# Performance work log

Hardware: AMD Instinct MI355X
Metric: run time of the kernel (lower is better)

## Reference

```python
import jax, jax.numpy as jnp
import numpy as np

N = 50000
E = 800000
IN_C = 256
NHID = 32
HEADS = 4
OUT_C = 64
HID = NHID * HEADS  # 128
SLOPE = 0.2


def setup_inputs() -> dict:
    key = jax.random.key(0)
    ks = jax.random.split(key, 16)
    s = lambda *d: 1.0 / np.sqrt(d[0])
    inp = {
        "x": jax.random.normal(ks[0], (N, IN_C), dtype=jnp.float32),
        "edge_index": jax.random.randint(ks[1], (2, E), 0, N, dtype=jnp.int64),
        # conv1: GATConv(IN_C, NHID, heads=HEADS, concat=True)
        "W1": jax.random.normal(ks[2], (IN_C, HEADS * NHID), dtype=jnp.float32) * s(IN_C),
        "att_src1": jax.random.normal(ks[3], (HEADS, NHID), dtype=jnp.float32) * s(NHID),
        "att_dst1": jax.random.normal(ks[4], (HEADS, NHID), dtype=jnp.float32) * s(NHID),
        "b1": jnp.zeros((HEADS * NHID,), dtype=jnp.float32),
        # conv2: GATConv(HID, OUT_C, heads=1, concat=False)
        "W2": jax.random.normal(ks[5], (HID, OUT_C), dtype=jnp.float32) * s(HID),
        "att_src2": jax.random.normal(ks[6], (1, OUT_C), dtype=jnp.float32) * s(OUT_C),
        "att_dst2": jax.random.normal(ks[7], (1, OUT_C), dtype=jnp.float32) * s(OUT_C),
        "b2": jnp.zeros((OUT_C,), dtype=jnp.float32),
        # res1: Linear(IN_C, HID)
        "res1_w": jax.random.normal(ks[8], (IN_C, HID), dtype=jnp.float32) * s(IN_C),
        "res1_b": jnp.zeros((HID,), dtype=jnp.float32),
        # fc: Linear(HID, OUT_C)
        "fc_w": jax.random.normal(ks[9], (HID, OUT_C), dtype=jnp.float32) * s(HID),
        "fc_b": jnp.zeros((OUT_C,), dtype=jnp.float32),
    }
    return inp


def leaky_relu(x, slope=SLOPE):
    return jnp.where(x >= 0, x, slope * x)


def gat_conv(x, edge_index, W, att_src, att_dst, bias, heads, out_c, concat):
    """PyG GATConv with default add_self_loops=True, negative_slope=0.2."""
    n = x.shape[0]
    loop = jnp.arange(n, dtype=edge_index.dtype)
    src = jnp.concatenate([edge_index[0], loop])  # [E+N]
    dst = jnp.concatenate([edge_index[1], loop])
    h = (x @ W).reshape(n, heads, out_c)          # [N,H,C]
    a_src = (h * att_src[None]).sum(-1)           # [N,H]
    a_dst = (h * att_dst[None]).sum(-1)
    alpha = leaky_relu(a_src[src] + a_dst[dst])   # [E+N,H]
    # segment softmax over destination nodes (every node has a self loop)
    amax = jax.ops.segment_max(alpha, dst, num_segments=n)
    expa = jnp.exp(alpha - amax[dst])
    denom = jax.ops.segment_sum(expa, dst, num_segments=n)
    alpha = expa / (denom[dst] + 1e-16)
    msg = alpha[:, :, None] * h[src]              # [E+N,H,C] irregular gather
    out = jax.ops.segment_sum(msg, dst, num_segments=n)  # scatter-add
    if concat:
        out = out.reshape(n, heads * out_c)
    else:
        out = out.mean(axis=1)
    return out + bias


def reference(x, edge_index, W1, att_src1, att_dst1, b1, W2, att_src2, att_dst2, b2,
              res1_w, res1_b, fc_w, fc_b):
    x_res = x @ res1_w + res1_b
    h = gat_conv(x, edge_index, W1, att_src1, att_dst1, b1, HEADS, NHID, True) + x_res
    h_res = h @ fc_w + fc_b
    h = leaky_relu(h)
    z = gat_conv(h, edge_index, W2, att_src2, att_dst2, b2, 1, OUT_C, False) + h_res
    z = leaky_relu(z)
    return z
```

## Files before the change

kernel.cpp:

```cpp
#include <hip/hip_runtime.h>

typedef __attribute__((ext_vector_type(8))) short short8;
typedef __attribute__((ext_vector_type(4))) float f32x4;

constexpr int BCAP = 4096;

__device__ __forceinline__ ushort rne_bf16(float f) {
  uint u = __float_as_uint(f);
  uint r = (u + 0x7FFFu + ((u >> 16) & 1u)) >> 16;
  return (ushort)r;
}
__device__ __forceinline__ float bf16_lo(uint pair) { return __uint_as_float(pair << 16); }
__device__ __forceinline__ float bf16_hi(uint pair) { return __uint_as_float(pair & 0xffff0000u); }
__device__ __forceinline__ float bf1(ushort v) { return __uint_as_float((uint)v << 16); }
__device__ __forceinline__ float lrelu(float a) { return a >= 0.f ? a : 0.2f * a; }

__device__ __forceinline__ uint lrelu_pair(uint pair) {
  float lo = lrelu(bf16_lo(pair));
  float hi = lrelu(bf16_hi(pair));
  return (uint)rne_bf16(lo) | ((uint)rne_bf16(hi) << 16);
}
__device__ __forceinline__ short8 lrelu_s8(short8 v) {
  uint4 u = *(uint4*)&v;
  u.x = lrelu_pair(u.x); u.y = lrelu_pair(u.y);
  u.z = lrelu_pair(u.z); u.w = lrelu_pair(u.w);
  return *(short8*)&u;
}
__device__ __forceinline__ float4 pack_bf8(float4 a, float4 b) {
  uint u0 = (uint)rne_bf16(a.x) | ((uint)rne_bf16(a.y) << 16);
  uint u1 = (uint)rne_bf16(a.z) | ((uint)rne_bf16(a.w) << 16);
  uint u2 = (uint)rne_bf16(b.x) | ((uint)rne_bf16(b.y) << 16);
  uint u3 = (uint)rne_bf16(b.z) | ((uint)rne_bf16(b.w) << 16);
  uint4 r; r.x = u0; r.y = u1; r.z = u2; r.w = u3;
  return *(float4*)&r;
}

__global__ __launch_bounds__(256) void prep_all_k(
    const int* __restrict__ ei, int E, int nEB,
    int* __restrict__ bcnt, uint2* __restrict__ tmp, int nbuck,
    const float* __restrict__ W1, const float* __restrict__ res1_w,
    const float* __restrict__ fc_w, const float* __restrict__ W2,
    ushort* __restrict__ Wt1, ushort* __restrict__ fcT, ushort* __restrict__ W2T)
{
  __shared__ int lcnt[400];
  __shared__ int gbase[400];
  const int tid = threadIdx.x, bid = blockIdx.x;
  const long gstride = (long)gridDim.x * 256;
  const long g0 = (long)bid * 256 + tid;

  if (bid < nEB) {
    for (int i = tid; i < nbuck; i += 256) lcnt[i] = 0;
    __syncthreads();
    const int ebase = bid * 4096;
    int srcs[16], dsts[16], rk[16];
#pragma unroll
    for (int i = 0; i < 16; ++i) {
      int e = ebase + i * 256 + tid;
      if (e < E) {
        srcs[i] = ei[e];
        dsts[i] = ei[E + e];
        rk[i] = atomicAdd(&lcnt[dsts[i] >> 7], 1);
      } else dsts[i] = -1;
    }
    __syncthreads();
    for (int b = tid; b < nbuck; b += 256)
      gbase[b] = lcnt[b] ? atomicAdd(&bcnt[b], lcnt[b]) : 0;
    __syncthreads();
#pragma unroll
    for (int i = 0; i < 16; ++i) {
      if (dsts[i] >= 0) {
        int b = dsts[i] >> 7;
        tmp[(size_t)b * BCAP + gbase[b] + rk[i]] = make_uint2((uint)srcs[i], (uint)dsts[i]);
      }
    }
  }

  for (long gi = g0; gi < 81920; gi += gstride) {
    const float* src; ushort* dst; int K, NO; long local;
    if (gi < 32768)            { src = W1;     dst = Wt1;          K = 256; NO = 128; local = gi; }
    else if (gi < 65536)       { src = res1_w; dst = Wt1 + 32768;  K = 256; NO = 128; local = gi - 32768; }
    else if (gi < 65536+8192)  { src = fc_w;   dst = fcT;          K = 128; NO = 64;  local = gi - 65536; }
    else                       { src = W2;     dst = W2T;          K = 128; NO = 64;  local = gi - 65536 - 8192; }
    int n = (int)(local / K), k = (int)(local % K);
    dst[local] = rne_bf16(src[(size_t)k * NO + n]);
  }
}

__global__ __launch_bounds__(512) void scan_buckets_k(const int* __restrict__ bcnt,
                                                      int* __restrict__ bbase,
                                                      int* __restrict__ offp,
                                                      int nbuck, int N) {
  __shared__ int sh[512];
  int tid = threadIdx.x;
  int v = (tid < nbuck) ? bcnt[tid] : 0;
  sh[tid] = v;
  __syncthreads();
  for (int o = 1; o < 512; o <<= 1) {
    int t = (tid >= o) ? sh[tid - o] : 0;
    __syncthreads();
    sh[tid] += t;
    __syncthreads();
  }
  if (tid < nbuck) bbase[tid] = sh[tid] - v;
  if (tid == nbuck - 1) { bbase[nbuck] = sh[tid]; offp[N] = sh[tid]; }
}

__global__ __launch_bounds__(512) void gemm1_k(
    const float* __restrict__ x, const ushort* __restrict__ Wt1,
    const float* __restrict__ res1_b,
    const float* __restrict__ att_s1, const float* __restrict__ att_d1,
    ushort* __restrict__ h1bf, ushort* __restrict__ xresbf,
    float* __restrict__ a_s, float* __restrict__ a_d,
    const uint2* __restrict__ tmp, const int* __restrict__ bcnt,
    const int* __restrict__ bbase, int* __restrict__ offp,
    int* __restrict__ csr, int nbuck, int M)
{
  constexpr int LDA = 72;
  __shared__ ushort smem[64 * LDA + 128 * LDA];
  const int bid = blockIdx.x, y = blockIdx.y, tid = threadIdx.x;
  ushort* As = smem;
  ushort* Bs = smem + 64 * LDA;
  const int w = tid >> 6, l = tid & 63;
  const int wr = w >> 2, wc = w & 3;
  const int l15 = l & 15, lg = l >> 4;
  const int row0 = bid * 64;
  const int srow = tid >> 3, sch = tid & 7;

  int gra = row0 + srow; if (gra >= M) gra = M - 1;
  const float*  Apf = x + (size_t)gra * 256 + sch * 8;
  const ushort* Bp  = Wt1 + ((size_t)y * 128 + srow) * 256 + sch * 8;

  f32x4 acc[2][2] = {};
  float4 raCa, raCb, rbC0, rbC1, raNa, raNb, rbN0, rbN1;
  raCa = *(const float4*)(Apf);
  raCb = *(const float4*)(Apf + 4);
  rbC0 = *(const float4*)(Bp);
  rbC1 = *(const float4*)(Bp + 64 * 256);

#pragma unroll
  for (int kt = 0; kt < 4; ++kt) {
    __syncthreads();
    *(float4*)&As[srow * LDA + sch * 8] = pack_bf8(raCa, raCb);
    *(float4*)&Bs[srow * LDA + sch * 8] = rbC0;
    *(float4*)&Bs[(64 + srow) * LDA + sch * 8] = rbC1;
    __syncthreads();
    if (kt < 3) {
      int k1 = (kt + 1) * 64;
      raNa = *(const float4*)(Apf + k1);
      raNb = *(const float4*)(Apf + k1 + 4);
      rbN0 = *(const float4*)(Bp + k1);
      rbN1 = *(const float4*)(Bp + 64 * 256 + k1);
    }
    short8 aF[2][2], bF[2][2];
#pragma unroll
    for (int m = 0; m < 2; ++m)
#pragma unroll
      for (int kk = 0; kk < 2; ++kk)
        aF[m][kk] = *(const short8*)&As[(wr * 32 + m * 16 + l15) * LDA + kk * 32 + lg * 8];
#pragma unroll
    for (int n = 0; n < 2; ++n)
#pragma unroll
      for (int kk = 0; kk < 2; ++kk)
        bF[n][kk] = *(const short8*)&Bs[(wc * 32 + n * 16 + l15) * LDA + kk * 32 + lg * 8];
#pragma unroll
    for (int m = 0; m < 2; ++m)
#pragma unroll
      for (int n = 0; n < 2; ++n)
#pragma unroll
        for (int kk = 0; kk < 2; ++kk)
          acc[m][n] = __builtin_amdgcn_mfma_f32_16x16x32_bf16(aF[m][kk], bF[n][kk], acc[m][n], 0, 0, 0);
    raCa = raNa; raCb = raNb; rbC0 = rbN0; rbC1 = rbN1;
  }
  __syncthreads();

  ushort* Cs = smem;
#pragma unroll
  for (int m = 0; m < 2; ++m)
#pragma unroll
    for (int n = 0; n < 2; ++n)
#pragma unroll
      for (int j = 0; j < 4; ++j) {
        int rl = wr * 32 + m * 16 + lg * 4 + j;
        int col = wc * 32 + n * 16 + l15;
        float v = acc[m][n][j] + (y ? res1_b[col] : 0.f);
        Cs[rl * 128 + col] = rne_bf16(v);
      }
  __syncthreads();

  if (y == 0) {
    int r = tid >> 3, s = tid & 7, h = s >> 1;
    int gr = row0 + r;
    float ps = 0.f, pd = 0.f;
#pragma unroll
    for (int i = 0; i < 16; ++i) {
      int col = s * 16 + i;
      float v = bf1(Cs[r * 128 + col]);
      ps += v * att_s1[h * 32 + (col & 31)];
      pd += v * att_d1[h * 32 + (col & 31)];
    }
    ps += __shfl_xor(ps, 1, 64);
    pd += __shfl_xor(pd, 1, 64);
    if (!(s & 1) && gr < M) { a_s[gr * 4 + h] = ps; a_d[gr * 4 + h] = pd; }
  }

  {
    ushort* out = y ? xresbf : h1bf;
#pragma unroll
    for (int idx = tid; idx < 1024; idx += 512) {
      int row = idx >> 4, c16 = idx & 15;
      int gr = row0 + row;
      if (gr < M)
        *(uint4*)&out[(size_t)gr * 128 + c16 * 8] = *(const uint4*)&Cs[row * 128 + c16 * 8];
    }
  }

  if (y == 1 && bid < nbuck) {
    __syncthreads();
    int* lcnt = (int*)smem;
    int* excl = lcnt + 128;
    const int vbase = bid * 128;
    const int nloc = ((vbase + 128 < M) ? 128 : M - vbase);
    const int cntb = bcnt[bid];
    const int bbase0 = bbase[bid];
    const uint2* bt = tmp + (size_t)bid * BCAP;
    if (tid < 128) lcnt[tid] = 0;
    __syncthreads();
    for (int e = tid; e < cntb; e += 512)
      atomicAdd(&lcnt[(int)bt[e].y - vbase], 1);
    __syncthreads();
    if (tid < 128) {
      int v = lcnt[tid];
      int sc = v;
#pragma unroll
      for (int o = 1; o < 64; o <<= 1) {
        int t = __shfl_up(sc, o, 64);
        if ((tid & 63) >= o) sc += t;
      }
      excl[tid] = sc - v;
    }
    __syncthreads();
    if (tid >= 64 && tid < 128) excl[tid] += excl[63] + lcnt[63];
    __syncthreads();
    if (tid < nloc) offp[vbase + tid] = bbase0 + excl[tid];
    if (tid < 128) lcnt[tid] = 0;
    __syncthreads();
    for (int e = tid; e < cntb; e += 512) {
      uint2 t = bt[e];
      int li = (int)t.y - vbase;
      int r = atomicAdd(&lcnt[li], 1);
      csr[bbase0 + excl[li] + r] = (int)t.x;
    }
  }
}

__global__ __launch_bounds__(512) void agg1_gemm2_k(
    const uint* __restrict__ h1u, const uint* __restrict__ xresu,
    const float* __restrict__ a_s1, const float* __restrict__ a_d1,
    const int* __restrict__ off, const int* __restrict__ csr,
    const float* __restrict__ b1,
    const ushort* __restrict__ fcT,
    const float* __restrict__ fc_b,
    const float* __restrict__ att_s2, const float* __restrict__ att_d2,
    ushort* __restrict__ hresb, ushort* __restrict__ h2bf,
    float* __restrict__ a_s2, float* __restrict__ a_d2, int n)
{
  constexpr int LDH = 136;
  __shared__ ushort smem[64 * LDH + 128 * LDH];
  ushort* hpreT = smem;
  ushort* Bs    = smem + 64 * LDH;

  const int tid = threadIdx.x;
  const int w = tid >> 6, l = tid & 63;
  const int l15 = l & 15, lg = l >> 4;
  const int d0 = blockIdx.x * 64;

#pragma unroll
  for (int c = tid; c < 2048; c += 512) {
    int row = c >> 4, ch = c & 15;
    *(uint4*)&Bs[row * LDH + ch * 8] = *(const uint4*)&fcT[(size_t)row * 128 + ch * 8];
  }

  const int h = l >> 4, c2 = l * 2;
  const int le = l & 15, hb = l & 48;
  for (int k = 0; k < 8; ++k) {
    int dl = w * 8 + k;
    int d = d0 + dl;
    if (d < n) {
      float adh = a_d1[d * 4 + h];
      float ws = __expf(lrelu(a_s1[d * 4 + h] + adh));
      uint pd = h1u[(size_t)d * 64 + l];
      float lsum = ws, accx = ws * bf16_lo(pd), accy = ws * bf16_hi(pd);

      int s0 = off[d], s1 = off[d + 1];
      int p = s0;
      for (; p + 16 <= s1; p += 16) {
        int idxv = csr[p + le];
        float wv = __expf(lrelu(a_s1[idxv * 4 + h] + adh));
        float wi[16]; int sv[16];
#pragma unroll
        for (int i = 0; i < 16; ++i) {
          wi[i] = __shfl(wv, hb + i, 64);
          sv[i] = __shfl(idxv, i, 64);
        }
#pragma unroll
        for (int i = 0; i < 16; ++i) {
          uint q = h1u[(size_t)sv[i] * 64 + l];
          lsum += wi[i];
          accx += wi[i] * bf16_lo(q);
          accy += wi[i] * bf16_hi(q);
        }
      }
      if (p < s1) {
        int rem = s1 - p;
        int jp = p + le;
        bool valid = jp < s1;
        int jc = valid ? jp : s1 - 1;
        int idxv = csr[jc];
        float wv = valid ? __expf(lrelu(a_s1[idxv * 4 + h] + adh)) : 0.f;
        for (int i = 0; i < rem; i += 4) {
#pragma unroll
          for (int j = 0; j < 4; ++j) {
            float wib = __shfl(wv, hb + i + j, 64);
            int svb = __shfl(idxv, i + j, 64);
            uint q = h1u[(size_t)svb * 64 + l];
            lsum += wib;
            accx += wib * bf16_lo(q);
            accy += wib * bf16_hi(q);
          }
        }
      }
      float inv = 1.f / (lsum + 1e-16f);
      uint xr = xresu[(size_t)d * 64 + l];
      float vx = accx * inv + b1[c2] + bf16_lo(xr);
      float vy = accy * inv + b1[c2 + 1] + bf16_hi(xr);
      *(uint*)&hpreT[dl * LDH + c2] = (uint)rne_bf16(vx) | ((uint)rne_bf16(vy) << 16);
    } else if (dl < 64) {
      *(uint*)&hpreT[dl * LDH + c2] = 0;
    }
  }
  __syncthreads();

  const int yh = w >> 2;
  const int wr = w & 3;
  f32x4 acc[4] = {};
#pragma unroll
  for (int kk = 0; kk < 4; ++kk) {
    short8 aF = *(const short8*)&hpreT[(wr * 16 + l15) * LDH + kk * 32 + lg * 8];
    if (yh) aF = lrelu_s8(aF);
#pragma unroll
    for (int nn = 0; nn < 4; ++nn) {
      short8 bF = *(const short8*)&Bs[(yh * 64 + nn * 16 + l15) * LDH + kk * 32 + lg * 8];
      acc[nn] = __builtin_amdgcn_mfma_f32_16x16x32_bf16(aF, bF, acc[nn], 0, 0, 0);
    }
  }
  __syncthreads();

  ushort* C0 = smem;
  ushort* C1 = smem + 4096;
#pragma unroll
  for (int nn = 0; nn < 4; ++nn)
#pragma unroll
    for (int j = 0; j < 4; ++j) {
      int rl = wr * 16 + lg * 4 + j;
      int col = nn * 16 + l15;
      float v = acc[nn][j] + (yh == 0 ? fc_b[col] : 0.f);
      (yh ? C1 : C0)[rl * 64 + col] = rne_bf16(v);
    }
  __syncthreads();

  {
    int r = tid >> 3, s = tid & 7;
    int d = d0 + r;
    float ps = 0.f, pdd = 0.f;
#pragma unroll
    for (int i = 0; i < 8; ++i) {
      int col = s * 8 + i;
      float v = bf1(C1[r * 64 + col]);
      ps += v * att_s2[col];
      pdd += v * att_d2[col];
    }
    ps += __shfl_xor(ps, 1, 64); pdd += __shfl_xor(pdd, 1, 64);
    ps += __shfl_xor(ps, 2, 64); pdd += __shfl_xor(pdd, 2, 64);
    ps += __shfl_xor(ps, 4, 64); pdd += __shfl_xor(pdd, 4, 64);
    if (s == 0 && d < n) { a_s2[d] = ps; a_d2[d] = pdd; }
  }

  {
    int row = tid >> 3, ch = tid & 7;
    int d = d0 + row;
    if (d < n) {
      *(uint4*)&hresb[(size_t)d * 64 + ch * 8] = *(const uint4*)&C0[row * 64 + ch * 8];
      *(uint4*)&h2bf[(size_t)d * 64 + ch * 8]  = *(const uint4*)&C1[row * 64 + ch * 8];
    }
  }
}

__global__ __launch_bounds__(256) void aggr2_k(const ushort* __restrict__ h2b,
                                               const ushort* __restrict__ hresb,
                                               const float* __restrict__ a_s,
                                               const float* __restrict__ a_d,
                                               const int* __restrict__ off,
                                               const int* __restrict__ csr,
                                               const float* __restrict__ b2,
                                               float* __restrict__ out, int n) {
  int w = threadIdx.x >> 6, l = threadIdx.x & 63;
  int d = blockIdx.x * 4 + w;
  if (d >= n) return;
  int le = l & 15;
  float adh = a_d[d];
  float ws = __expf(lrelu(a_s[d] + adh));
  float lsum = ws;
  float acc = ws * bf1(h2b[(size_t)d * 64 + l]);

  int s0 = off[d], s1 = off[d + 1];
  int p = s0;
  for (; p + 16 <= s1; p += 16) {
    int idxv = csr[p + le];
    float wv = __expf(lrelu(a_s[idxv] + adh));
    float wi[16]; int sv[16];
#pragma unroll
    for (int i = 0; i < 16; ++i) {
      wi[i] = __shfl(wv, i, 64);
      sv[i] = __shfl(idxv, i, 64);
    }
#pragma unroll
    for (int i = 0; i < 16; ++i) {
      float fv = bf1(h2b[(size_t)sv[i] * 64 + l]);
      lsum += wi[i];
      acc += wi[i] * fv;
    }
  }
  if (p < s1) {
    int rem = s1 - p;
    int jp = p + le;
    bool valid = jp < s1;
    int jc = valid ? jp : s1 - 1;
    int idxv = csr[jc];
    float wv = valid ? __expf(lrelu(a_s[idxv] + adh)) : 0.f;
    for (int i = 0; i < rem; i += 4) {
#pragma unroll
      for (int j = 0; j < 4; ++j) {
        float wib = __shfl(wv, i + j, 64);
        int svb = __shfl(idxv, i + j, 64);
        float fv = bf1(h2b[(size_t)svb * 64 + l]);
        lsum += wib;
        acc += wib * fv;
      }
    }
  }
  float inv = 1.f / (lsum + 1e-16f);
  float z = acc * inv + b2[l] + bf1(hresb[(size_t)d * 64 + l]);
  out[(size_t)d * 64 + l] = lrelu(z);
}

extern "C" void kernel_launch(void* const* d_in, const int* in_sizes, int n_in,
                              void* d_out, int out_size, void* d_ws, size_t ws_size,
                              hipStream_t stream) {
  const float* x        = (const float*)d_in[0];
  const int*   ei       = (const int*)d_in[1];
  const float* W1       = (const float*)d_in[2];
  const float* att_src1 = (const float*)d_in[3];
  const float* att_dst1 = (const float*)d_in[4];
  const float* b1       = (const float*)d_in[5];
  const float* W2       = (const float*)d_in[6];
  const float* att_src2 = (const float*)d_in[7];
  const float* att_dst2 = (const float*)d_in[8];
  const float* b2       = (const float*)d_in[9];
  const float* res1_w   = (const float*)d_in[10];
  const float* res1_b   = (const float*)d_in[11];
  const float* fc_w     = (const float*)d_in[12];
  const float* fc_b     = (const float*)d_in[13];
  float* out = (float*)d_out;

  const int N = in_sizes[0] / 256;
  const int E = in_sizes[1] / 2;
  const int nbuck = (N + 127) / 128;
  const int nEB = (E + 4095) / 4096;

  ushort* h1bf   = (ushort*)d_ws;
  ushort* xresbf = h1bf + (size_t)N * 128;
  ushort* hresb  = xresbf + (size_t)N * 128;
  ushort* h2bf   = hresb + (size_t)N * 64;
  float*  as1    = (float*)(h2bf + (size_t)N * 64);
  float*  ad1    = as1 + (size_t)N * 4;
  float*  as2    = ad1 + (size_t)N * 4;
  float*  ad2    = as2 + (size_t)N;
  ushort* Wt1    = (ushort*)(ad2 + (size_t)N);
  ushort* fcT    = Wt1 + 256 * 256;
  ushort* W2T    = fcT + 64 * 128;
  int* offp      = (int*)(W2T + 64 * 128);
  int* csr       = offp + N + 1;
  int* bcnt      = csr + E;
  int* bbase     = bcnt + 512;
  uint2* tmp     = (uint2*)(((uintptr_t)(bbase + 520) + 7) & ~(uintptr_t)7);

  const int ngemm = (N + 63) / 64;

  hipMemsetAsync(bcnt, 0, 512 * 4, stream);
  prep_all_k<<<nEB, 256, 0, stream>>>(ei, E, nEB, bcnt, tmp, nbuck,
                                      W1, res1_w, fc_w, W2, Wt1, fcT, W2T);
  scan_buckets_k<<<1, 512, 0, stream>>>(bcnt, bbase, offp, nbuck, N);

  gemm1_k<<<dim3(ngemm, 2), 512, 0, stream>>>(x, Wt1, res1_b, att_src1, att_dst1,
                                              h1bf, xresbf, as1, ad1,
                                              tmp, bcnt, bbase, offp, csr, nbuck, N);

  agg1_gemm2_k<<<ngemm, 512, 0, stream>>>(
      (const uint*)h1bf, (const uint*)xresbf, as1, ad1, offp, csr, b1,
      fcT, fc_b, att_src2, att_dst2, hresb, h2bf, as2, ad2, N);

  aggr2_k<<<(N + 3) / 4, 256, 0, stream>>>(h2bf, hresb, as2, ad2, offp, csr, b2, out, N);
}
```

Measured before the change: 166.7 us.

## Prefetch next neighbor chunk in aggregation loops and read fc weights from global

Both aggregation kernels now issue the next 16-edge chunk's CSR index and attention-weight loads before processing the current chunk. This software-pipelines the dependent csr -> a_s -> h gather latency chain and merges the tail handling into a single loop. The fused agg1/gemm2 kernel also stops staging the fc/W2 weight matrix in shared memory and reads the MFMA B fragments straight from global memory. That cuts LDS use, which may allow more blocks per CU, at the cost of repeated global (likely cached) weight loads and extra register pressure from the prefetched values.

```diff
diff --git a/kernel.cpp b/kernel.cpp
--- a/kernel.cpp
+++ b/kernel.cpp
@@ -265,20 +265,11 @@
     float* __restrict__ a_s2, float* __restrict__ a_d2, int n)
 {
   constexpr int LDH = 136;
-  __shared__ ushort smem[64 * LDH + 128 * LDH];
-  ushort* hpreT = smem;
-  ushort* Bs    = smem + 64 * LDH;
-
+  __shared__ ushort hpreT[64 * LDH];
   const int tid = threadIdx.x;
   const int w = tid >> 6, l = tid & 63;
   const int l15 = l & 15, lg = l >> 4;
   const int d0 = blockIdx.x * 64;
-
-#pragma unroll
-  for (int c = tid; c < 2048; c += 512) {
-    int row = c >> 4, ch = c & 15;
-    *(uint4*)&Bs[row * LDH + ch * 8] = *(const uint4*)&fcT[(size_t)row * 128 + ch * 8];
-  }
 
   const int h = l >> 4, c2 = l * 2;
   const int le = l & 15, hb = l & 48;
@@ -286,55 +277,65 @@
     int dl = w * 8 + k;
     int d = d0 + dl;
     if (d < n) {
+      int s0 = off[d], s1 = off[d + 1];
       float adh = a_d1[d * 4 + h];
+      int p = s0;
+      int idxN = 0; float wN = 0.f;
+      if (p < s1) {
+        int jp = p + le;
+        int jc = jp < s1 ? jp : s1 - 1;
+        idxN = csr[jc];
+        wN = (jp < s1) ? __expf(lrelu(a_s1[idxN * 4 + h] + adh)) : 0.f;
+      }
       float ws = __expf(lrelu(a_s1[d * 4 + h] + adh));
       uint pd = h1u[(size_t)d * 64 + l];
       float lsum = ws, accx = ws * bf16_lo(pd), accy = ws * bf16_hi(pd);
 
-      int s0 = off[d], s1 = off[d + 1];
-      int p = s0;
-      for (; p + 16 <= s1; p += 16) {
-        int idxv = csr[p + le];
-        float wv = __expf(lrelu(a_s1[idxv * 4 + h] + adh));
-        float wi[16]; int sv[16];
-#pragma unroll
-        for (int i = 0; i < 16; ++i) {
-          wi[i] = __shfl(wv, hb + i, 64);
-          sv[i] = __shfl(idxv, i, 64);
+      while (p < s1) {
+        int idxC = idxN; float wC = wN;
+        int pn = p + 16;
+        if (pn < s1) {
+          int jp = pn + le;
+          int jc = jp < s1 ? jp : s1 - 1;
+          idxN = csr[jc];
+          wN = (jp < s1) ? __expf(lrelu(a_s1[idxN * 4 + h] + adh)) : 0.f;
         }
-#pragma unroll
-        for (int i = 0; i < 16; ++i) {
-          uint q = h1u[(size_t)sv[i] * 64 + l];
-          lsum += wi[i];
-          accx += wi[i] * bf16_lo(q);
-          accy += wi[i] * bf16_hi(q);
-        }
-      }
-      if (p < s1) {
-        int rem = s1 - p;
-        int jp = p + le;
-        bool valid = jp < s1;
-        int jc = valid ? jp : s1 - 1;
-        int idxv = csr[jc];
-        float wv = valid ? __expf(lrelu(a_s1[idxv * 4 + h] + adh)) : 0.f;
-        for (int i = 0; i < rem; i += 4) {
-#pragma unroll
-          for (int j = 0; j < 4; ++j) {
-            float wib = __shfl(wv, hb + i + j, 64);
-            int svb = __shfl(idxv, i + j, 64);
-            uint q = h1u[(size_t)svb * 64 + l];
-            lsum += wib;
-            accx += wib * bf16_lo(q);
-            accy += wib * bf16_hi(q);
+        if (s1 - p >= 16) {
+          float wi[16]; int sv[16];
+#pragma unroll
+          for (int i = 0; i < 16; ++i) {
+            wi[i] = __shfl(wC, hb + i, 64);
+            sv[i] = __shfl(idxC, i, 64);
+          }
+#pragma unroll
+          for (int i = 0; i < 16; ++i) {
+            uint q = h1u[(size_t)sv[i] * 64 + l];
+            lsum += wi[i];
+            accx += wi[i] * bf16_lo(q);
+            accy += wi[i] * bf16_hi(q);
+          }
+        } else {
+          int rem = s1 - p;
+          for (int i = 0; i < rem; i += 4) {
+#pragma unroll
+            for (int j = 0; j < 4; ++j) {
+              float wib = __shfl(wC, hb + i + j, 64);
+              int svb = __shfl(idxC, i + j, 64);
+              uint q = h1u[(size_t)svb * 64 + l];
+              lsum += wib;
+              accx += wib * bf16_lo(q);
+              accy += wib * bf16_hi(q);
+            }
           }
         }
+        p = pn;
       }
       float inv = 1.f / (lsum + 1e-16f);
       uint xr = xresu[(size_t)d * 64 + l];
       float vx = accx * inv + b1[c2] + bf16_lo(xr);
       float vy = accy * inv + b1[c2 + 1] + bf16_hi(xr);
       *(uint*)&hpreT[dl * LDH + c2] = (uint)rne_bf16(vx) | ((uint)rne_bf16(vy) << 16);
-    } else if (dl < 64) {
+    } else {
       *(uint*)&hpreT[dl * LDH + c2] = 0;
     }
   }
@@ -342,6 +343,7 @@
 
   const int yh = w >> 2;
   const int wr = w & 3;
+  const ushort* Bg = fcT + (size_t)yh * 64 * 128;
   f32x4 acc[4] = {};
 #pragma unroll
   for (int kk = 0; kk < 4; ++kk) {
@@ -349,14 +351,14 @@
     if (yh) aF = lrelu_s8(aF);
 #pragma unroll
     for (int nn = 0; nn < 4; ++nn) {
-      short8 bF = *(const short8*)&Bs[(yh * 64 + nn * 16 + l15) * LDH + kk * 32 + lg * 8];
+      short8 bF = *(const short8*)&Bg[(size_t)(nn * 16 + l15) * 128 + kk * 32 + lg * 8];
       acc[nn] = __builtin_amdgcn_mfma_f32_16x16x32_bf16(aF, bF, acc[nn], 0, 0, 0);
     }
   }
   __syncthreads();
 
-  ushort* C0 = smem;
-  ushort* C1 = smem + 4096;
+  ushort* C0 = hpreT;
+  ushort* C1 = hpreT + 4096;
 #pragma unroll
   for (int nn = 0; nn < 4; ++nn)
 #pragma unroll
@@ -407,46 +409,58 @@
   int d = blockIdx.x * 4 + w;
   if (d >= n) return;
   int le = l & 15;
+  int s0 = off[d], s1 = off[d + 1];
   float adh = a_d[d];
+
+  int p = s0;
+  int idxN = 0; float wN = 0.f;
+  if (p < s1) {
+    int jp = p + le;
+    int jc = jp < s1 ? jp : s1 - 1;
+    idxN = csr[jc];
+    wN = (jp < s1) ? __expf(lrelu(a_s[idxN] + adh)) : 0.f;
+  }
+
   float ws = __expf(lrelu(a_s[d] + adh));
   float lsum = ws;
   float acc = ws * bf1(h2b[(size_t)d * 64 + l]);
 
-  int s0 = off[d], s1 = off[d + 1];
-  int p = s0;
-  for (; p + 16 <= s1; p += 16) {
-    int idxv = csr[p + le];
-    float wv = __expf(lrelu(a_s[idxv] + adh));
-    float wi[16]; int sv[16];
-#pragma unroll
-    for (int i = 0; i < 16; ++i) {
-      wi[i] = __shfl(wv, i, 64);
-      sv[i] = __shfl(idxv, i, 64);
-    }
-#pragma unroll
-    for (int i = 0; i < 16; ++i) {
-      float fv = bf1(h2b[(size_t)sv[i] * 64 + l]);
-      lsum += wi[i];
-      acc += wi[i] * fv;
-    }
-  }
-  if (p < s1) {
-    int rem = s1 - p;
-    int jp = p + le;
-    bool valid = jp < s1;
-    int jc = valid ? jp : s1 - 1;
-    int idxv = csr[jc];
-    float wv = valid ? __expf(lrelu(a_s[idxv] + adh)) : 0.f;
-    for (int i = 0; i < rem; i += 4) {
-#pragma unroll
-      for (int j = 0; j < 4; ++j) {
-        float wib = __shfl(wv, i + j, 64);
-        int svb = __shfl(idxv, i + j, 64);
-        float fv = bf1(h2b[(size_t)svb * 64 + l]);
-        lsum += wib;
-        acc += wib * fv;
-      }
-    }
+  while (p < s1) {
+    int idxC = idxN; float wC = wN;
+    int pn = p + 16;
+    if (pn < s1) {
+      int jp = pn + le;
+      int jc = jp < s1 ? jp : s1 - 1;
+      idxN = csr[jc];
+      wN = (jp < s1) ? __expf(lrelu(a_s[idxN] + adh)) : 0.f;
+    }
+    if (s1 - p >= 16) {
+      float wi[16]; int sv[16];
+#pragma unroll
+      for (int i = 0; i < 16; ++i) {
+        wi[i] = __shfl(wC, i, 64);
+        sv[i] = __shfl(idxC, i, 64);
+      }
+#pragma unroll
+      for (int i = 0; i < 16; ++i) {
+        float fv = bf1(h2b[(size_t)sv[i] * 64 + l]);
+        lsum += wi[i];
+        acc += wi[i] * fv;
+      }
+    } else {
+      int rem = s1 - p;
+      for (int i = 0; i < rem; i += 4) {
+#pragma unroll
+        for (int j = 0; j < 4; ++j) {
+          float wib = __shfl(wC, i + j, 64);
+          int svb = __shfl(idxC, i + j, 64);
+          float fv = bf1(h2b[(size_t)svb * 64 + l]);
+          lsum += wib;
+          acc += wib * fv;
+        }
+      }
+    }
+    p = pn;
   }
   float inv = 1.f / (lsum + 1e-16f);
   float z = acc * inv + b2[l] + bf1(hresb[(size_t)d * 64 + l]);
```

Result: slower. 175.9 us (+5.6%).
